# Kernel tuning notes

Hardware: AMD Instinct MI355X
Metric: run time of the kernel (lower is better)

## Reference

```python
import jax, jax.numpy as jnp
import numpy as np

N = 100000   # nodes
E = 1600000  # edges (avg degree 16)
D = 128      # feature dim
L = 2        # nr_layers


def setup_inputs() -> dict:
    key = jax.random.key(0)
    k0, k1, k2, k3, k4 = jax.random.split(key, 5)
    x = jax.random.normal(k0, (N, D), dtype=jnp.float32)
    edge_index = jax.random.randint(k1, (2, E), 0, N, dtype=jnp.int32)
    edge_weight = jax.random.uniform(k2, (E,), dtype=jnp.float32)
    scale = 1.0 / np.sqrt(D)
    W_self = jax.random.normal(k3, (L, D, D), dtype=jnp.float32) * scale
    W_neigh = jax.random.normal(k4, (L, D, D), dtype=jnp.float32) * scale
    bias = jnp.zeros((L, D), dtype=jnp.float32)
    return {"x": x, "edge_index": edge_index, "edge_weight": edge_weight,
            "W_self": W_self, "W_neigh": W_neigh, "bias": bias}


def reference(x, edge_index, edge_weight, W_self, W_neigh, bias):
    src, dst = edge_index[0], edge_index[1]
    n = x.shape[0]
    # mean-aggregation denominator: number of incoming edges per node
    deg = jax.ops.segment_sum(jnp.ones_like(edge_weight), dst, num_segments=n)
    deg = jnp.maximum(deg, 1.0)[:, None]  # [N,1]
    nl = W_self.shape[0]
    for l in range(nl):
        msg = edge_weight[:, None] * x[src]                       # [E,D] gather
        agg = jax.ops.segment_sum(msg, dst, num_segments=n) / deg  # [N,D] scatter
        x = agg @ W_neigh[l] + x @ W_self[l] + bias[l]
        x = jax.nn.relu(x) if l < nl - 1 else jax.nn.sigmoid(x)
    return x
```

## Files before the change

kernel.cpp:

```cpp
#include <hip/hip_runtime.h>
#include <math.h>


#define D 128
#define BK_SHIFT 9
#define BK_NODES 512
#define CAP 10240
#define CH1 4096

typedef unsigned int uint;
typedef unsigned short ushort;
typedef __attribute__((ext_vector_type(8))) short short8;
typedef __attribute__((ext_vector_type(4))) float f32x4;
typedef __attribute__((ext_vector_type(2))) float f32x2;

__device__ __forceinline__ float bf_lo(uint u) { return __uint_as_float(u << 16); }
__device__ __forceinline__ float bf_hi(uint u) { return __uint_as_float(u & 0xffff0000u); }
__device__ __forceinline__ ushort f2bf(float f) {
    uint u = __float_as_uint(f);
    u += 0x7fffu + ((u >> 16) & 1u);
    return (ushort)(u >> 16);
}
__device__ __forceinline__ uint pack2bf(float lo, float hi) {
    return (uint)f2bf(lo) | ((uint)f2bf(hi) << 16);
}

__global__ __launch_bounds__(256) void k_prep(
    const float* __restrict__ x, uint* __restrict__ xb, int n8,
    const float* __restrict__ Wn, const float* __restrict__ Ws,
    ushort* __restrict__ wt, int wtotal,
    const int* __restrict__ src, const int* __restrict__ dst,
    const float* __restrict__ w, int E,
    int* __restrict__ bcur, int2* __restrict__ bedge,
    int nbConv, int nbW)
{
    __shared__ int h[256];
    __shared__ int gbase[256];
    const int t = threadIdx.x;
    const int bid = blockIdx.x;

    if (bid < nbConv) {
        int i = bid * 256 + t;
        if (i >= n8) return;
        const float4* p = reinterpret_cast<const float4*>(x + (size_t)i * 8);
        float4 a = p[0], b = p[1];
        uint4 o;
        o.x = pack2bf(a.x, a.y);
        o.y = pack2bf(a.z, a.w);
        o.z = pack2bf(b.x, b.y);
        o.w = pack2bf(b.z, b.w);
        reinterpret_cast<uint4*>(xb)[i] = o;
        return;
    }
    if (bid < nbConv + nbW) {
        int idx = (bid - nbConv) * 256 + t;
        if (idx >= wtotal) return;
        int l = idx >> 15;
        int j = (idx >> 8) & 127;
        int k = idx & 255;
        float v = (k < 128) ? Wn[(size_t)l * 16384 + (size_t)k * 128 + j]
                            : Ws[(size_t)l * 16384 + (size_t)(k - 128) * 128 + j];
        wt[idx] = f2bf(v);
        return;
    }

    h[t] = 0;
    __syncthreads();
    const int base0 = (bid - nbConv - nbW) * CH1;
    uint pk[16]; float wr[16]; int br[16];
#pragma unroll
    for (int j = 0; j < 16; ++j) {
        int i = base0 + j * 256 + t;
        br[j] = -1;
        if (i < E) {
            int d = dst[i];
            int b = d >> BK_SHIFT;
            int r = atomicAdd(&h[b], 1);
            pk[j] = (uint)src[i] | ((uint)(d & (BK_NODES - 1)) << 17);
            wr[j] = w[i];
            br[j] = (b << 16) | r;
        }
    }
    __syncthreads();
    if (h[t] > 0) gbase[t] = atomicAdd(&bcur[t], h[t]);
    __syncthreads();
#pragma unroll
    for (int j = 0; j < 16; ++j) {
        if (br[j] >= 0) {
            int b = br[j] >> 16, r = br[j] & 0xffff;
            int slot = gbase[b] + r;
            if (slot < CAP)
                bedge[(size_t)b * CAP + slot] = make_int2((int)pk[j], __float_as_int(wr[j]));
        }
    }
}

__global__ __launch_bounds__(512) void k_sort2(
    const int2* __restrict__ bedge, const int* __restrict__ bcnt,
    int N, int2* __restrict__ rsdeg, int2* __restrict__ srcw)
{
    __shared__ int h[512];
    __shared__ int sa[512];
    __shared__ int sb[512];
    __shared__ int cur[512];
    const int t = threadIdx.x;
    const int b = blockIdx.x;
    const int gb = b * CAP;
    int cnt = bcnt[b];
    if (cnt > CAP) cnt = CAP;
    const int lo = b * BK_NODES;
    h[t] = 0;
    __syncthreads();
    for (int i = t; i < cnt; i += 512) {
        atomicAdd(&h[((uint)bedge[gb + i].x >> 17) & 511], 1);
    }
    __syncthreads();
    sa[t] = h[t];
    __syncthreads();
    int* sin = sa; int* sout = sb;
    for (int off = 1; off < 512; off <<= 1) {
        int v = sin[t];
        if (t >= off) v += sin[t - off];
        sout[t] = v;
        __syncthreads();
        int* tmp = sin; sin = sout; sout = tmp;
    }
    const int ex = sin[t] - h[t];
    cur[t] = ex;
    if (lo + t < N) rsdeg[lo + t] = make_int2(gb + ex, h[t]);
    __syncthreads();
    for (int i = t; i < cnt; i += 512) {
        int2 pe = bedge[gb + i];
        int n9 = ((uint)pe.x >> 17) & 511;
        int off = atomicAdd(&cur[n9], 1);
        srcw[gb + off] = make_int2(pe.x & 0x1FFFF, pe.y);
    }
}

__global__ __launch_bounds__(256, 8) void k_agg(
    const uint* __restrict__ xbf,
    const int2* __restrict__ srcw,
    const int2* __restrict__ rsdeg,
    uint* __restrict__ agg, int N)
{
    const int tid = threadIdx.x;
    const int wv = tid >> 6;
    const int lane = tid & 63;
    const int node = blockIdx.x * 4 + wv;
    if (node >= N) return;
    const int q = lane >> 4;
    const int c16 = lane & 15;
    const int2 rd = rsdeg[node];
    const int st = rd.x;
    const int num = rd.y;
    const int en = st + num;

    f32x2 a2[4];
#pragma unroll
    for (int j = 0; j < 4; ++j) a2[j] = (f32x2){0.f, 0.f};

#pragma unroll 4
    for (int e = st + q; e < en; e += 4) {
        const int2 sw = srcw[e];
        const float wv_ = __int_as_float(sw.y);
        const f32x2 w2 = {wv_, wv_};
        const uint4 v = reinterpret_cast<const uint4*>(xbf + (size_t)sw.x * 64)[c16];
        f32x2 p0 = {bf_lo(v.x), bf_hi(v.x)};
        f32x2 p1 = {bf_lo(v.y), bf_hi(v.y)};
        f32x2 p2 = {bf_lo(v.z), bf_hi(v.z)};
        f32x2 p3 = {bf_lo(v.w), bf_hi(v.w)};
        a2[0] = __builtin_elementwise_fma(w2, p0, a2[0]);
        a2[1] = __builtin_elementwise_fma(w2, p1, a2[1]);
        a2[2] = __builtin_elementwise_fma(w2, p2, a2[2]);
        a2[3] = __builtin_elementwise_fma(w2, p3, a2[3]);
    }

    float a[8];
    a[0] = a2[0].x; a[1] = a2[0].y;
    a[2] = a2[1].x; a[3] = a2[1].y;
    a[4] = a2[2].x; a[5] = a2[2].y;
    a[6] = a2[3].x; a[7] = a2[3].y;
#pragma unroll
    for (int j = 0; j < 8; ++j) {
        a[j] += __shfl_xor(a[j], 16);
        a[j] += __shfl_xor(a[j], 32);
    }

    if (q == 0) {
        const float invd = 1.0f / (float)(num > 1 ? num : 1);
        uint4 o;
        o.x = pack2bf(a[0] * invd, a[1] * invd);
        o.y = pack2bf(a[2] * invd, a[3] * invd);
        o.z = pack2bf(a[4] * invd, a[5] * invd);
        o.w = pack2bf(a[6] * invd, a[7] * invd);
        reinterpret_cast<uint4*>(agg + (size_t)node * 64)[c16] = o;
    }
}

template <int ACT, int OUTB>
__global__ __launch_bounds__(256) void k_gemm_mfma(
    const uint* __restrict__ aggb, const uint* __restrict__ xb,
    const uint* __restrict__ wt,
    const float* __restrict__ bias, void* __restrict__ xout, int N)
{
    const int tid = threadIdx.x;
    const int lane = tid & 63;
    const int wv = tid >> 6;
    const int wm = wv >> 1, wn = wv & 1;
    const int l16 = lane & 15;
    const int lq = lane >> 4;
    const int rowbase = blockIdx.x * 64 + wm * 32;
    const int colbase = wn * 64;

    short8 afrag[2][8];
#pragma unroll
    for (int mt = 0; mt < 2; ++mt) {
        int row = rowbase + mt * 16 + l16;
        if (row >= N) row = N - 1;
        const uint* arow = aggb + (size_t)row * 64;
        const uint* xrow = xb + (size_t)row * 64;
#pragma unroll
        for (int kk = 0; kk < 8; ++kk) {
            const uint* srcrow = (kk < 4) ? arow : xrow;
            uint4 u = *reinterpret_cast<const uint4*>(srcrow + (kk & 3) * 16 + lq * 4);
            afrag[mt][kk] = *reinterpret_cast<short8*>(&u);
        }
    }

#pragma unroll
    for (int nt = 0; nt < 4; ++nt) {
        const int col = colbase + nt * 16 + l16;
        const uint* wrow = wt + (size_t)col * 128;
        f32x4 acc0 = {0.f, 0.f, 0.f, 0.f};
        f32x4 acc1 = {0.f, 0.f, 0.f, 0.f};
#pragma unroll
        for (int kk = 0; kk < 8; ++kk) {
            uint4 u = *reinterpret_cast<const uint4*>(wrow + kk * 16 + lq * 4);
            short8 bfrag = *reinterpret_cast<short8*>(&u);
            acc0 = __builtin_amdgcn_mfma_f32_16x16x32_bf16(afrag[0][kk], bfrag, acc0, 0, 0, 0);
            acc1 = __builtin_amdgcn_mfma_f32_16x16x32_bf16(afrag[1][kk], bfrag, acc1, 0, 0, 0);
        }
        const float bv = bias[col];
#pragma unroll
        for (int mt = 0; mt < 2; ++mt) {
            const f32x4 acc = mt ? acc1 : acc0;
#pragma unroll
            for (int r = 0; r < 4; ++r) {
                int row = rowbase + mt * 16 + lq * 4 + r;
                if (row < N) {
                    float v = acc[r] + bv;
                    if (ACT == 0) v = fmaxf(v, 0.f);
                    else          v = 1.f / (1.f + __expf(-v));
                    if (OUTB) ((ushort*)xout)[(size_t)row * D + col] = f2bf(v);
                    else      ((float*)xout)[(size_t)row * D + col] = v;
                }
            }
        }
    }
}

extern "C" void kernel_launch(void* const* d_in, const int* in_sizes, int n_in,
                              void* d_out, int out_size, void* d_ws, size_t ws_size,
                              hipStream_t stream) {
    const float* x      = (const float*)d_in[0];
    const int*   ei     = (const int*)d_in[1];
    const float* ew     = (const float*)d_in[2];
    const float* W_self = (const float*)d_in[3];
    const float* W_neigh= (const float*)d_in[4];
    const float* bias   = (const float*)d_in[5];
    float* out = (float*)d_out;

    const int N = in_sizes[0] / D;
    const int E = in_sizes[2];
    const int L = in_sizes[5] / D;
    const int B = (N + BK_NODES - 1) >> BK_SHIFT;

    const int* src = ei;
    const int* dst = ei + E;

    char* p = (char*)d_ws;
    auto carve = [&](size_t bytes) -> void* {
        void* r = (void*)p;
        p += (bytes + 255) & ~(size_t)255;
        return r;
    };
    int*   bcur   = (int*)carve(256 * 4);
    int2*  bedge  = (int2*)carve((size_t)B * CAP * 8);
    int2*  srcw   = (int2*)carve((size_t)B * CAP * 8);
    int2*  rsdeg  = (int2*)carve((size_t)N * 8);
    uint*  xb     = (uint*)carve((size_t)N * (D / 2) * 4);
    uint*  aggb   = (uint*)carve((size_t)N * (D / 2) * 4);
    uint*  hb     = (uint*)carve((size_t)N * (D / 2) * 4);
    uint*  wtbl   = (uint*)carve((size_t)L * 128 * 128 * 4);

    hipMemsetAsync(bcur, 0, 256 * 4, stream);
    const int n8 = N * D / 8;
    const int wtotal = L * 32768;
    const int nbConv = (n8 + 255) / 256;
    const int nbW = (wtotal + 255) / 256;
    const int nbSort = (E + CH1 - 1) / CH1;
    k_prep<<<nbConv + nbW + nbSort, 256, 0, stream>>>(
        x, xb, n8, W_neigh, W_self, (ushort*)wtbl, wtotal,
        src, dst, ew, E, bcur, bedge, nbConv, nbW);
    k_sort2<<<B, 512, 0, stream>>>(bedge, bcur, N, rsdeg, srcw);

    const int nblk_agg  = (N + 3) / 4;
    const int nblk_gemm = (N + 63) / 64;
    const uint* cur = xb;
    for (int l = 0; l < L; ++l) {
        const uint* wtl = wtbl + (size_t)l * 128 * 128;
        const float* bl = bias + (size_t)l * D;

        k_agg<<<nblk_agg, 256, 0, stream>>>(cur, srcw, rsdeg, aggb, N);
        if (l < L - 1) {
            k_gemm_mfma<0, 1><<<nblk_gemm, 256, 0, stream>>>(aggb, cur, wtl, bl, hb, N);
            cur = hb;
        } else {
            k_gemm_mfma<1, 0><<<nblk_gemm, 256, 0, stream>>>(aggb, cur, wtl, bl, out, N);
        }
    }
}
```

Baseline: 267.2 us.

## Fuse neighbor aggregation into MFMA GEMM kernel via swizzled LDS tile

Each 64-row block now aggregates its own nodes' neighbor features into a swizzled shared-memory tile and then runs the bf16 MFMA GEMM from it. This removes the separate aggregation kernel and the round trip of the agg buffer through global memory. Bucket size drops from 512 to 256 nodes (CAP 6144, 512 buckets), and src indices are pre-shifted into byte offsets so the gather skips a multiply. In exchange, each wave handles 16 nodes serially, so fewer independent gathers are in flight and occupancy may suffer from the LDS tile and launch bounds.

```diff
diff --git a/kernel.cpp b/kernel.cpp
--- a/kernel.cpp
+++ b/kernel.cpp
@@ -3,9 +3,9 @@
 
 
 #define D 128
-#define BK_SHIFT 9
-#define BK_NODES 512
-#define CAP 10240
+#define BK_SHIFT 8
+#define BK_NODES 256
+#define CAP 6144
 #define CH1 4096
 
 typedef unsigned int uint;
@@ -34,8 +34,8 @@
     int* __restrict__ bcur, int2* __restrict__ bedge,
     int nbConv, int nbW)
 {
-    __shared__ int h[256];
-    __shared__ int gbase[256];
+    __shared__ int h[512];
+    __shared__ int gbase[512];
     const int t = threadIdx.x;
     const int bid = blockIdx.x;
 
@@ -64,7 +64,7 @@
         return;
     }
 
-    h[t] = 0;
+    h[t] = 0; h[t + 256] = 0;
     __syncthreads();
     const int base0 = (bid - nbConv - nbW) * CH1;
     uint pk[16]; float wr[16]; int br[16];
@@ -82,7 +82,8 @@
         }
     }
     __syncthreads();
-    if (h[t] > 0) gbase[t] = atomicAdd(&bcur[t], h[t]);
+    for (int u = t; u < 512; u += 256)
+        if (h[u] > 0) gbase[u] = atomicAdd(&bcur[u], h[u]);
     __syncthreads();
 #pragma unroll
     for (int j = 0; j < 16; ++j) {
@@ -95,30 +96,30 @@
     }
 }
 
-__global__ __launch_bounds__(512) void k_sort2(
+__global__ __launch_bounds__(256) void k_sort2(
     const int2* __restrict__ bedge, const int* __restrict__ bcnt,
     int N, int2* __restrict__ rsdeg, int2* __restrict__ srcw)
 {
-    __shared__ int h[512];
-    __shared__ int sa[512];
-    __shared__ int sb[512];
-    __shared__ int cur[512];
+    __shared__ int h[256];
+    __shared__ int sa[256];
+    __shared__ int sb[256];
+    __shared__ int cur[256];
     const int t = threadIdx.x;
     const int b = blockIdx.x;
     const int gb = b * CAP;
     int cnt = bcnt[b];
     if (cnt > CAP) cnt = CAP;
-    const int lo = b * BK_NODES;
+    const int lo = b << BK_SHIFT;
     h[t] = 0;
     __syncthreads();
-    for (int i = t; i < cnt; i += 512) {
-        atomicAdd(&h[((uint)bedge[gb + i].x >> 17) & 511], 1);
+    for (int i = t; i < cnt; i += 256) {
+        atomicAdd(&h[((uint)bedge[gb + i].x >> 17) & 255], 1);
     }
     __syncthreads();
     sa[t] = h[t];
     __syncthreads();
     int* sin = sa; int* sout = sb;
-    for (int off = 1; off < 512; off <<= 1) {
+    for (int off = 1; off < 256; off <<= 1) {
         int v = sin[t];
         if (t >= off) v += sin[t - off];
         sout[t] = v;
@@ -129,100 +130,102 @@
     cur[t] = ex;
     if (lo + t < N) rsdeg[lo + t] = make_int2(gb + ex, h[t]);
     __syncthreads();
-    for (int i = t; i < cnt; i += 512) {
+    for (int i = t; i < cnt; i += 256) {
         int2 pe = bedge[gb + i];
-        int n9 = ((uint)pe.x >> 17) & 511;
-        int off = atomicAdd(&cur[n9], 1);
-        srcw[gb + off] = make_int2(pe.x & 0x1FFFF, pe.y);
-    }
-}
-
-__global__ __launch_bounds__(256, 8) void k_agg(
+        int n8i = ((uint)pe.x >> 17) & 255;
+        int off = atomicAdd(&cur[n8i], 1);
+        srcw[gb + off] = make_int2((pe.x & 0x1FFFF) << 8, pe.y);
+    }
+}
+
+template <int ACT, int OUTB>
+__global__ __launch_bounds__(256, 4) void k_layer(
     const uint* __restrict__ xbf,
     const int2* __restrict__ srcw,
     const int2* __restrict__ rsdeg,
-    uint* __restrict__ agg, int N)
-{
-    const int tid = threadIdx.x;
-    const int wv = tid >> 6;
-    const int lane = tid & 63;
-    const int node = blockIdx.x * 4 + wv;
-    if (node >= N) return;
-    const int q = lane >> 4;
-    const int c16 = lane & 15;
-    const int2 rd = rsdeg[node];
-    const int st = rd.x;
-    const int num = rd.y;
-    const int en = st + num;
-
-    f32x2 a2[4];
-#pragma unroll
-    for (int j = 0; j < 4; ++j) a2[j] = (f32x2){0.f, 0.f};
-
-#pragma unroll 4
-    for (int e = st + q; e < en; e += 4) {
-        const int2 sw = srcw[e];
-        const float wv_ = __int_as_float(sw.y);
-        const f32x2 w2 = {wv_, wv_};
-        const uint4 v = reinterpret_cast<const uint4*>(xbf + (size_t)sw.x * 64)[c16];
-        f32x2 p0 = {bf_lo(v.x), bf_hi(v.x)};
-        f32x2 p1 = {bf_lo(v.y), bf_hi(v.y)};
-        f32x2 p2 = {bf_lo(v.z), bf_hi(v.z)};
-        f32x2 p3 = {bf_lo(v.w), bf_hi(v.w)};
-        a2[0] = __builtin_elementwise_fma(w2, p0, a2[0]);
-        a2[1] = __builtin_elementwise_fma(w2, p1, a2[1]);
-        a2[2] = __builtin_elementwise_fma(w2, p2, a2[2]);
-        a2[3] = __builtin_elementwise_fma(w2, p3, a2[3]);
-    }
-
-    float a[8];
-    a[0] = a2[0].x; a[1] = a2[0].y;
-    a[2] = a2[1].x; a[3] = a2[1].y;
-    a[4] = a2[2].x; a[5] = a2[2].y;
-    a[6] = a2[3].x; a[7] = a2[3].y;
-#pragma unroll
-    for (int j = 0; j < 8; ++j) {
-        a[j] += __shfl_xor(a[j], 16);
-        a[j] += __shfl_xor(a[j], 32);
-    }
-
-    if (q == 0) {
-        const float invd = 1.0f / (float)(num > 1 ? num : 1);
-        uint4 o;
-        o.x = pack2bf(a[0] * invd, a[1] * invd);
-        o.y = pack2bf(a[2] * invd, a[3] * invd);
-        o.z = pack2bf(a[4] * invd, a[5] * invd);
-        o.w = pack2bf(a[6] * invd, a[7] * invd);
-        reinterpret_cast<uint4*>(agg + (size_t)node * 64)[c16] = o;
-    }
-}
-
-template <int ACT, int OUTB>
-__global__ __launch_bounds__(256) void k_gemm_mfma(
-    const uint* __restrict__ aggb, const uint* __restrict__ xb,
     const uint* __restrict__ wt,
     const float* __restrict__ bias, void* __restrict__ xout, int N)
 {
+    __shared__ uint sAgg[64 * 64];
     const int tid = threadIdx.x;
     const int lane = tid & 63;
     const int wv = tid >> 6;
+    const int brow = blockIdx.x * 64;
+
+    {
+        const int q = lane >> 4;
+        const int c16 = lane & 15;
+        for (int i = 0; i < 16; ++i) {
+            const int lr = wv * 16 + i;
+            const int node = brow + lr;
+            f32x2 a2[4];
+#pragma unroll
+            for (int j = 0; j < 4; ++j) a2[j] = (f32x2){0.f, 0.f};
+            int st = 0, num = 0;
+            if (node < N) { int2 rd = rsdeg[node]; st = rd.x; num = rd.y; }
+            const int en = st + num;
+#pragma unroll 4
+            for (int e = st + q; e < en; e += 4) {
+                const int2 sw = srcw[e];
+                const float wv_ = __int_as_float(sw.y);
+                const f32x2 w2 = {wv_, wv_};
+                const uint4 v = *reinterpret_cast<const uint4*>(
+                    (const char*)xbf + (uint)sw.x + (c16 << 4));
+                f32x2 p0 = {bf_lo(v.x), bf_hi(v.x)};
+                f32x2 p1 = {bf_lo(v.y), bf_hi(v.y)};
+                f32x2 p2 = {bf_lo(v.z), bf_hi(v.z)};
+                f32x2 p3 = {bf_lo(v.w), bf_hi(v.w)};
+                a2[0] = __builtin_elementwise_fma(w2, p0, a2[0]);
+                a2[1] = __builtin_elementwise_fma(w2, p1, a2[1]);
+                a2[2] = __builtin_elementwise_fma(w2, p2, a2[2]);
+                a2[3] = __builtin_elementwise_fma(w2, p3, a2[3]);
+            }
+            float a[8];
+            a[0] = a2[0].x; a[1] = a2[0].y;
+            a[2] = a2[1].x; a[3] = a2[1].y;
+            a[4] = a2[2].x; a[5] = a2[2].y;
+            a[6] = a2[3].x; a[7] = a2[3].y;
+#pragma unroll
+            for (int j = 0; j < 8; ++j) {
+                a[j] += __shfl_xor(a[j], 16);
+                a[j] += __shfl_xor(a[j], 32);
+            }
+            if (q == 0 && node < N) {
+                const float invd = 1.0f / (float)(num > 1 ? num : 1);
+                uint4 o;
+                o.x = pack2bf(a[0] * invd, a[1] * invd);
+                o.y = pack2bf(a[2] * invd, a[3] * invd);
+                o.z = pack2bf(a[4] * invd, a[5] * invd);
+                o.w = pack2bf(a[6] * invd, a[7] * invd);
+                const int g = c16 ^ (lr & 7);
+                *reinterpret_cast<uint4*>(&sAgg[lr * 64 + (g << 2)]) = o;
+            }
+        }
+    }
+    __syncthreads();
+
     const int wm = wv >> 1, wn = wv & 1;
     const int l16 = lane & 15;
     const int lq = lane >> 4;
-    const int rowbase = blockIdx.x * 64 + wm * 32;
+    const int rowbase = brow + wm * 32;
     const int colbase = wn * 64;
 
     short8 afrag[2][8];
 #pragma unroll
     for (int mt = 0; mt < 2; ++mt) {
-        int row = rowbase + mt * 16 + l16;
-        if (row >= N) row = N - 1;
-        const uint* arow = aggb + (size_t)row * 64;
-        const uint* xrow = xb + (size_t)row * 64;
-#pragma unroll
-        for (int kk = 0; kk < 8; ++kk) {
-            const uint* srcrow = (kk < 4) ? arow : xrow;
-            uint4 u = *reinterpret_cast<const uint4*>(srcrow + (kk & 3) * 16 + lq * 4);
+        const int lr = wm * 32 + mt * 16 + l16;
+        int grow = brow + lr;
+        if (grow >= N) grow = N - 1;
+        const uint* xrow = xbf + (size_t)grow * 64;
+#pragma unroll
+        for (int kk = 0; kk < 4; ++kk) {
+            const int g = (kk * 4 + lq) ^ (lr & 7);
+            uint4 u = *reinterpret_cast<const uint4*>(&sAgg[lr * 64 + (g << 2)]);
+            afrag[mt][kk] = *reinterpret_cast<short8*>(&u);
+        }
+#pragma unroll
+        for (int kk = 4; kk < 8; ++kk) {
+            uint4 u = *reinterpret_cast<const uint4*>(xrow + (kk - 4) * 16 + lq * 4);
             afrag[mt][kk] = *reinterpret_cast<short8*>(&u);
         }
     }
@@ -284,16 +287,15 @@
         p += (bytes + 255) & ~(size_t)255;
         return r;
     };
-    int*   bcur   = (int*)carve(256 * 4);
+    int*   bcur   = (int*)carve(512 * 4);
     int2*  bedge  = (int2*)carve((size_t)B * CAP * 8);
     int2*  srcw   = (int2*)carve((size_t)B * CAP * 8);
     int2*  rsdeg  = (int2*)carve((size_t)N * 8);
     uint*  xb     = (uint*)carve((size_t)N * (D / 2) * 4);
-    uint*  aggb   = (uint*)carve((size_t)N * (D / 2) * 4);
     uint*  hb     = (uint*)carve((size_t)N * (D / 2) * 4);
     uint*  wtbl   = (uint*)carve((size_t)L * 128 * 128 * 4);
 
-    hipMemsetAsync(bcur, 0, 256 * 4, stream);
+    hipMemsetAsync(bcur, 0, 512 * 4, stream);
     const int n8 = N * D / 8;
     const int wtotal = L * 32768;
     const int nbConv = (n8 + 255) / 256;
@@ -302,21 +304,18 @@
     k_prep<<<nbConv + nbW + nbSort, 256, 0, stream>>>(
         x, xb, n8, W_neigh, W_self, (ushort*)wtbl, wtotal,
         src, dst, ew, E, bcur, bedge, nbConv, nbW);
-    k_sort2<<<B, 512, 0, stream>>>(bedge, bcur, N, rsdeg, srcw);
-
-    const int nblk_agg  = (N + 3) / 4;
-    const int nblk_gemm = (N + 63) / 64;
+    k_sort2<<<B, 256, 0, stream>>>(bedge, bcur, N, rsdeg, srcw);
+
+    const int nblk = (N + 63) / 64;
     const uint* cur = xb;
     for (int l = 0; l < L; ++l) {
         const uint* wtl = wtbl + (size_t)l * 128 * 128;
         const float* bl = bias + (size_t)l * D;
-
-        k_agg<<<nblk_agg, 256, 0, stream>>>(cur, srcw, rsdeg, aggb, N);
         if (l < L - 1) {
-            k_gemm_mfma<0, 1><<<nblk_gemm, 256, 0, stream>>>(aggb, cur, wtl, bl, hb, N);
+            k_layer<0, 1><<<nblk, 256, 0, stream>>>(cur, srcw, rsdeg, wtl, bl, hb, N);
             cur = hb;
         } else {
-            k_gemm_mfma<1, 0><<<nblk_gemm, 256, 0, stream>>>(aggb, cur, wtl, bl, out, N);
-        }
-    }
-}
+            k_layer<1, 0><<<nblk, 256, 0, stream>>>(cur, srcw, rsdeg, wtl, bl, out, N);
+        }
+    }
+}
```

Measured after the change: 315.2 us. +18.0%, slower.

## Switch features and weights from bf16 to fp16 with packed-half aggregation

Applied to the files above, without the earlier changes.

Converts stored features, weights and edge weights from bf16 to fp16 (round-toward-zero packed conversion). Aggregation now accumulates in packed half2 FMAs instead of fp32, and does the cross-quarter shuffles and the degree normalisation in half. The source index is pre-shifted into a byte offset so no multiply is needed. The GEMM uses the f16 MFMA. This cuts ALU and unpack work in the gather loop, but accumulating up to ~16+ terms in fp16 adds rounding error and overflow risk.

```diff
diff --git a/kernel.cpp b/kernel.cpp
--- a/kernel.cpp
+++ b/kernel.cpp
@@ -10,23 +10,32 @@
 
 typedef unsigned int uint;
 typedef unsigned short ushort;
-typedef __attribute__((ext_vector_type(8))) short short8;
+typedef __attribute__((ext_vector_type(2))) _Float16 h2;
+typedef __attribute__((ext_vector_type(8))) _Float16 half8;
 typedef __attribute__((ext_vector_type(4))) float f32x4;
-typedef __attribute__((ext_vector_type(2))) float f32x2;
-
-__device__ __forceinline__ float bf_lo(uint u) { return __uint_as_float(u << 16); }
-__device__ __forceinline__ float bf_hi(uint u) { return __uint_as_float(u & 0xffff0000u); }
-__device__ __forceinline__ ushort f2bf(float f) {
-    uint u = __float_as_uint(f);
-    u += 0x7fffu + ((u >> 16) & 1u);
-    return (ushort)(u >> 16);
-}
-__device__ __forceinline__ uint pack2bf(float lo, float hi) {
-    return (uint)f2bf(lo) | ((uint)f2bf(hi) << 16);
+
+__device__ __forceinline__ uint pkrtz(float lo, float hi) {
+    auto v = __builtin_amdgcn_cvt_pkrtz(lo, hi);
+    union { decltype(v) h; uint u; } c;
+    c.h = v;
+    return c.u;
+}
+__device__ __forceinline__ ushort f2h(float f) {
+    return (ushort)(pkrtz(f, f) & 0xffffu);
+}
+__device__ __forceinline__ h2 u2h(uint u) {
+    union { uint u; h2 h; } c;
+    c.u = u;
+    return c.h;
+}
+__device__ __forceinline__ uint h2u(h2 h) {
+    union { h2 h; uint u; } c;
+    c.h = h;
+    return c.u;
 }
 
 __global__ __launch_bounds__(256) void k_prep(
-    const float* __restrict__ x, uint* __restrict__ xb, int n8,
+    const float* __restrict__ x, uint* __restrict__ xh, int n8,
     const float* __restrict__ Wn, const float* __restrict__ Ws,
     ushort* __restrict__ wt, int wtotal,
     const int* __restrict__ src, const int* __restrict__ dst,
@@ -45,11 +54,11 @@
         const float4* p = reinterpret_cast<const float4*>(x + (size_t)i * 8);
         float4 a = p[0], b = p[1];
         uint4 o;
-        o.x = pack2bf(a.x, a.y);
-        o.y = pack2bf(a.z, a.w);
-        o.z = pack2bf(b.x, b.y);
-        o.w = pack2bf(b.z, b.w);
-        reinterpret_cast<uint4*>(xb)[i] = o;
+        o.x = pkrtz(a.x, a.y);
+        o.y = pkrtz(a.z, a.w);
+        o.z = pkrtz(b.x, b.y);
+        o.w = pkrtz(b.z, b.w);
+        reinterpret_cast<uint4*>(xh)[i] = o;
         return;
     }
     if (bid < nbConv + nbW) {
@@ -60,7 +69,7 @@
         int k = idx & 255;
         float v = (k < 128) ? Wn[(size_t)l * 16384 + (size_t)k * 128 + j]
                             : Ws[(size_t)l * 16384 + (size_t)(k - 128) * 128 + j];
-        wt[idx] = f2bf(v);
+        wt[idx] = f2h(v);
         return;
     }
 
@@ -108,7 +117,7 @@
     const int gb = b * CAP;
     int cnt = bcnt[b];
     if (cnt > CAP) cnt = CAP;
-    const int lo = b * BK_NODES;
+    const int lo = b << BK_SHIFT;
     h[t] = 0;
     __syncthreads();
     for (int i = t; i < cnt; i += 512) {
@@ -133,12 +142,13 @@
         int2 pe = bedge[gb + i];
         int n9 = ((uint)pe.x >> 17) & 511;
         int off = atomicAdd(&cur[n9], 1);
-        srcw[gb + off] = make_int2(pe.x & 0x1FFFF, pe.y);
+        float wv = __int_as_float(pe.y);
+        srcw[gb + off] = make_int2((pe.x & 0x1FFFF) << 8, (int)pkrtz(wv, wv));
     }
 }
 
 __global__ __launch_bounds__(256, 8) void k_agg(
-    const uint* __restrict__ xbf,
+    const uint* __restrict__ xh,
     const int2* __restrict__ srcw,
     const int2* __restrict__ rsdeg,
     uint* __restrict__ agg, int N)
@@ -155,51 +165,43 @@
     const int num = rd.y;
     const int en = st + num;
 
-    f32x2 a2[4];
-#pragma unroll
-    for (int j = 0; j < 4; ++j) a2[j] = (f32x2){0.f, 0.f};
+    h2 a2[4];
+#pragma unroll
+    for (int j = 0; j < 4; ++j) a2[j] = u2h(0u);
 
 #pragma unroll 4
     for (int e = st + q; e < en; e += 4) {
         const int2 sw = srcw[e];
-        const float wv_ = __int_as_float(sw.y);
-        const f32x2 w2 = {wv_, wv_};
-        const uint4 v = reinterpret_cast<const uint4*>(xbf + (size_t)sw.x * 64)[c16];
-        f32x2 p0 = {bf_lo(v.x), bf_hi(v.x)};
-        f32x2 p1 = {bf_lo(v.y), bf_hi(v.y)};
-        f32x2 p2 = {bf_lo(v.z), bf_hi(v.z)};
-        f32x2 p3 = {bf_lo(v.w), bf_hi(v.w)};
-        a2[0] = __builtin_elementwise_fma(w2, p0, a2[0]);
-        a2[1] = __builtin_elementwise_fma(w2, p1, a2[1]);
-        a2[2] = __builtin_elementwise_fma(w2, p2, a2[2]);
-        a2[3] = __builtin_elementwise_fma(w2, p3, a2[3]);
-    }
-
-    float a[8];
-    a[0] = a2[0].x; a[1] = a2[0].y;
-    a[2] = a2[1].x; a[3] = a2[1].y;
-    a[4] = a2[2].x; a[5] = a2[2].y;
-    a[6] = a2[3].x; a[7] = a2[3].y;
-#pragma unroll
-    for (int j = 0; j < 8; ++j) {
-        a[j] += __shfl_xor(a[j], 16);
-        a[j] += __shfl_xor(a[j], 32);
+        const h2 w2 = u2h((uint)sw.y);
+        const uint4 v = *reinterpret_cast<const uint4*>(
+            (const char*)xh + (uint)sw.x + (c16 << 4));
+        a2[0] = __builtin_elementwise_fma(w2, u2h(v.x), a2[0]);
+        a2[1] = __builtin_elementwise_fma(w2, u2h(v.y), a2[1]);
+        a2[2] = __builtin_elementwise_fma(w2, u2h(v.z), a2[2]);
+        a2[3] = __builtin_elementwise_fma(w2, u2h(v.w), a2[3]);
+    }
+
+#pragma unroll
+    for (int j = 0; j < 4; ++j) {
+        a2[j] = a2[j] + u2h(__shfl_xor(h2u(a2[j]), 16));
+        a2[j] = a2[j] + u2h(__shfl_xor(h2u(a2[j]), 32));
     }
 
     if (q == 0) {
         const float invd = 1.0f / (float)(num > 1 ? num : 1);
+        const h2 iv = u2h(pkrtz(invd, invd));
         uint4 o;
-        o.x = pack2bf(a[0] * invd, a[1] * invd);
-        o.y = pack2bf(a[2] * invd, a[3] * invd);
-        o.z = pack2bf(a[4] * invd, a[5] * invd);
-        o.w = pack2bf(a[6] * invd, a[7] * invd);
+        o.x = h2u(a2[0] * iv);
+        o.y = h2u(a2[1] * iv);
+        o.z = h2u(a2[2] * iv);
+        o.w = h2u(a2[3] * iv);
         reinterpret_cast<uint4*>(agg + (size_t)node * 64)[c16] = o;
     }
 }
 
 template <int ACT, int OUTB>
 __global__ __launch_bounds__(256) void k_gemm_mfma(
-    const uint* __restrict__ aggb, const uint* __restrict__ xb,
+    const uint* __restrict__ aggh, const uint* __restrict__ xh,
     const uint* __restrict__ wt,
     const float* __restrict__ bias, void* __restrict__ xout, int N)
 {
@@ -212,18 +214,18 @@
     const int rowbase = blockIdx.x * 64 + wm * 32;
     const int colbase = wn * 64;
 
-    short8 afrag[2][8];
+    half8 afrag[2][8];
 #pragma unroll
     for (int mt = 0; mt < 2; ++mt) {
         int row = rowbase + mt * 16 + l16;
         if (row >= N) row = N - 1;
-        const uint* arow = aggb + (size_t)row * 64;
-        const uint* xrow = xb + (size_t)row * 64;
+        const uint* arow = aggh + (size_t)row * 64;
+        const uint* xrow = xh + (size_t)row * 64;
 #pragma unroll
         for (int kk = 0; kk < 8; ++kk) {
             const uint* srcrow = (kk < 4) ? arow : xrow;
             uint4 u = *reinterpret_cast<const uint4*>(srcrow + (kk & 3) * 16 + lq * 4);
-            afrag[mt][kk] = *reinterpret_cast<short8*>(&u);
+            afrag[mt][kk] = *reinterpret_cast<half8*>(&u);
         }
     }
 
@@ -236,9 +238,9 @@
 #pragma unroll
         for (int kk = 0; kk < 8; ++kk) {
             uint4 u = *reinterpret_cast<const uint4*>(wrow + kk * 16 + lq * 4);
-            short8 bfrag = *reinterpret_cast<short8*>(&u);
-            acc0 = __builtin_amdgcn_mfma_f32_16x16x32_bf16(afrag[0][kk], bfrag, acc0, 0, 0, 0);
-            acc1 = __builtin_amdgcn_mfma_f32_16x16x32_bf16(afrag[1][kk], bfrag, acc1, 0, 0, 0);
+            half8 bfrag = *reinterpret_cast<half8*>(&u);
+            acc0 = __builtin_amdgcn_mfma_f32_16x16x32_f16(afrag[0][kk], bfrag, acc0, 0, 0, 0);
+            acc1 = __builtin_amdgcn_mfma_f32_16x16x32_f16(afrag[1][kk], bfrag, acc1, 0, 0, 0);
         }
         const float bv = bias[col];
 #pragma unroll
@@ -251,7 +253,7 @@
                     float v = acc[r] + bv;
                     if (ACT == 0) v = fmaxf(v, 0.f);
                     else          v = 1.f / (1.f + __expf(-v));
-                    if (OUTB) ((ushort*)xout)[(size_t)row * D + col] = f2bf(v);
+                    if (OUTB) ((ushort*)xout)[(size_t)row * D + col] = f2h(v);
                     else      ((float*)xout)[(size_t)row * D + col] = v;
                 }
             }
@@ -288,35 +290,35 @@
     int2*  bedge  = (int2*)carve((size_t)B * CAP * 8);
     int2*  srcw   = (int2*)carve((size_t)B * CAP * 8);
     int2*  rsdeg  = (int2*)carve((size_t)N * 8);
-    uint*  xb     = (uint*)carve((size_t)N * (D / 2) * 4);
-    uint*  aggb   = (uint*)carve((size_t)N * (D / 2) * 4);
+    uint*  xh     = (uint*)carve((size_t)N * (D / 2) * 4);
+    uint*  aggh   = (uint*)carve((size_t)N * (D / 2) * 4);
     uint*  hb     = (uint*)carve((size_t)N * (D / 2) * 4);
     uint*  wtbl   = (uint*)carve((size_t)L * 128 * 128 * 4);
 
-    hipMemsetAsync(bcur, 0, 256 * 4, stream);
+    (void)hipMemsetAsync(bcur, 0, 256 * 4, stream);
     const int n8 = N * D / 8;
     const int wtotal = L * 32768;
     const int nbConv = (n8 + 255) / 256;
     const int nbW = (wtotal + 255) / 256;
     const int nbSort = (E + CH1 - 1) / CH1;
     k_prep<<<nbConv + nbW + nbSort, 256, 0, stream>>>(
-        x, xb, n8, W_neigh, W_self, (ushort*)wtbl, wtotal,
+        x, xh, n8, W_neigh, W_self, (ushort*)wtbl, wtotal,
         src, dst, ew, E, bcur, bedge, nbConv, nbW);
     k_sort2<<<B, 512, 0, stream>>>(bedge, bcur, N, rsdeg, srcw);
 
     const int nblk_agg  = (N + 3) / 4;
     const int nblk_gemm = (N + 63) / 64;
-    const uint* cur = xb;
+    const uint* cur = xh;
     for (int l = 0; l < L; ++l) {
         const uint* wtl = wtbl + (size_t)l * 128 * 128;
         const float* bl = bias + (size_t)l * D;
 
-        k_agg<<<nblk_agg, 256, 0, stream>>>(cur, srcw, rsdeg, aggb, N);
+        k_agg<<<nblk_agg, 256, 0, stream>>>(cur, srcw, rsdeg, aggh, N);
         if (l < L - 1) {
-            k_gemm_mfma<0, 1><<<nblk_gemm, 256, 0, stream>>>(aggb, cur, wtl, bl, hb, N);
+            k_gemm_mfma<0, 1><<<nblk_gemm, 256, 0, stream>>>(aggh, cur, wtl, bl, hb, N);
             cur = hb;
         } else {
-            k_gemm_mfma<1, 0><<<nblk_gemm, 256, 0, stream>>>(aggb, cur, wtl, bl, out, N);
-        }
-    }
-}
+            k_gemm_mfma<1, 0><<<nblk_gemm, 256, 0, stream>>>(aggh, cur, wtl, bl, out, N);
+        }
+    }
+}
```

Measured after the change: 264.1 us. Within noise of the previous version (-1.1%).
